# Kernel tuning notes

Measured on AMD Instinct MI355X. Metric: run time of the kernel, lower is better.

## Reference

```python
import jax, jax.numpy as jnp
import numpy as np

HEADS = 8
DIM_HEAD = 64
DIM = 512
KERNEL = 33
SCALE = DIM_HEAD ** -0.5


def setup_inputs() -> dict:
    key = jax.random.key(0)
    k1, k2, k3, k4, k5, k6 = jax.random.split(key, 6)
    b, n = 2, 2048
    inner = HEADS * DIM_HEAD
    x = jax.random.normal(k1, (b, n, DIM), dtype=jnp.float32)
    mask = jax.random.uniform(k2, (b, n)) < 0.9
    W_qkv = jax.random.normal(k3, (DIM, inner * 3), dtype=jnp.float32) / np.sqrt(DIM)
    W_out = jax.random.normal(k4, (inner, DIM), dtype=jnp.float32) / np.sqrt(inner)
    b_out = jax.random.normal(k5, (DIM,), dtype=jnp.float32) * 0.01
    # depthwise Conv2d(heads, heads, (K,1), groups=heads) weight: (O=heads, I/groups=1, K, 1)
    conv_w = jax.random.normal(k6, (HEADS, 1, KERNEL, 1), dtype=jnp.float32) / np.sqrt(KERNEL)
    return {"x": x, "mask": mask, "W_qkv": W_qkv, "W_out": W_out,
            "b_out": b_out, "conv_w": conv_w}


def reference(x, mask, W_qkv, W_out, b_out, conv_w):
    b, n, _ = x.shape
    h, d = HEADS, DIM_HEAD
    qkv = (x @ W_qkv).reshape(b, n, 3, h, d)          # chunk(3) then (h d) split
    q = qkv[:, :, 0].transpose(0, 2, 1, 3)            # b h n d
    k = qkv[:, :, 1].transpose(0, 2, 1, 3)
    v = qkv[:, :, 2].transpose(0, 2, 1, 3)
    dots = jnp.einsum('bhid,bhjd->bhij', q, k) * SCALE
    mask_value = -jnp.finfo(dots.dtype).max
    dots = jnp.where(mask[:, None, None, :], dots, mask_value)
    attn = jax.nn.softmax(dots, axis=-1)
    out = jnp.einsum('bhij,bhjd->bhid', attn, v)      # b h n d
    # depthwise residual conv over sequence axis (height), per head
    pad = KERNEL // 2
    res = jax.lax.conv_general_dilated(
        v, conv_w, window_strides=(1, 1), padding=((pad, pad), (0, 0)),
        dimension_numbers=('NCHW', 'OIHW', 'NCHW'), feature_group_count=h)
    out = out + res
    out = out.transpose(0, 2, 1, 3).reshape(b, n, h * d)  # b n (h d)
    out = out @ W_out + b_out
    out = jnp.where(mask[:, :, None], out, 0.0)
    return out
```

## Files before the change

### kernel.cpp

```cpp
#include <hip/hip_runtime.h>
#include <float.h>

#define BATCH 2
#define SEQ   2048
#define HEADS 8
#define DHEAD 64
#define DIMM  512
#define NQKV  1536
#define QSCALE_L2 (0.125f * 1.44269504f)

#define QKV_ELEMS ((size_t)BATCH * HEADS * SEQ * DHEAD)

typedef __bf16 bf16x8 __attribute__((ext_vector_type(8)));
typedef short  s16x4  __attribute__((ext_vector_type(4)));
typedef float  f32x4  __attribute__((ext_vector_type(4)));

#if __has_builtin(__builtin_amdgcn_exp2f)
#define EXP2F __builtin_amdgcn_exp2f
#else
#define EXP2F exp2f
#endif

__device__ __forceinline__ unsigned short bfbits(float f) {
  __bf16 h = (__bf16)f;
  return *(unsigned short*)&h;
}
__device__ __forceinline__ float bf2f(unsigned short u) {
  return __uint_as_float((unsigned)u << 16);
}
__device__ __forceinline__ unsigned cvtpk(float a, float b) {
  unsigned r;
  asm("v_cvt_pk_bf16_f32 %0, %1, %2" : "=v"(r) : "v"(a), "v"(b));
  return r;
}
__device__ __forceinline__ f32x4 mfma16(s16x4 a, s16x4 b, f32x4 c) {
#if __has_builtin(__builtin_amdgcn_mfma_f32_16x16x16bf16_1k)
  return __builtin_amdgcn_mfma_f32_16x16x16bf16_1k(a, b, c, 0, 0, 0);
#else
  f32x4 d;
  asm("v_mfma_f32_16x16x16_bf16 %0, %1, %2, %3" : "=v"(d) : "v"(a), "v"(b), "v"(c));
  return d;
#endif
}

__device__ __forceinline__ void transpose_tile_dev(
    const float* __restrict__ W, unsigned short* __restrict__ Wt,
    int K, int N, int n0, int k0, int t, float T[64][65]) {
  {
    int r0 = t >> 4, c4 = t & 15;
#pragma unroll
    for (int rr = 0; rr < 4; ++rr) {
      int r = r0 + rr * 16;
      float4 v = *(const float4*)(W + (size_t)(k0 + r) * N + n0 + c4 * 4);
      T[r][c4 * 4 + 0] = v.x; T[r][c4 * 4 + 1] = v.y;
      T[r][c4 * 4 + 2] = v.z; T[r][c4 * 4 + 3] = v.w;
    }
  }
  __syncthreads();
  {
    int n = t >> 2, kc = t & 3;
    union { unsigned short u[16]; int4 v[2]; } p;
#pragma unroll
    for (int i = 0; i < 16; ++i) p.u[i] = bfbits(T[kc * 16 + i][n]);
    int4* dst = (int4*)(Wt + (size_t)(n0 + n) * K + k0 + kc * 16);
    dst[0] = p.v[0]; dst[1] = p.v[1];
  }
}

__global__ __launch_bounds__(256) void prep_all(
    const float* __restrict__ X, const void* __restrict__ mraw,
    const float* __restrict__ Wqkv, const float* __restrict__ Wout,
    unsigned short* __restrict__ Xbf, float* __restrict__ maskf,
    unsigned short* __restrict__ Wtq, unsigned short* __restrict__ Wto,
    unsigned* __restrict__ kmaxn) {
  __shared__ float T[64][65];
  __shared__ int f_bf16, f_f32, f_gt1, f_oddnz;
  const int b = blockIdx.x;
  const int t = threadIdx.x;
  if (b < 1024) {
    size_t i = ((size_t)b * 256 + t) * 8;
    float4 a0 = *(const float4*)(X + i);
    float4 a1 = *(const float4*)(X + i + 4);
    union { unsigned short u[8]; int4 v; } pk;
    pk.u[0] = bfbits(a0.x); pk.u[1] = bfbits(a0.y);
    pk.u[2] = bfbits(a0.z); pk.u[3] = bfbits(a0.w);
    pk.u[4] = bfbits(a1.x); pk.u[5] = bfbits(a1.y);
    pk.u[6] = bfbits(a1.z); pk.u[7] = bfbits(a1.w);
    *(int4*)(Xbf + i) = pk.v;
  } else if (b < 1216) {
    int bb2 = b - 1024;
    transpose_tile_dev(Wqkv, Wtq, DIMM, NQKV, (bb2 % 24) * 64, (bb2 / 24) * 64, t, T);
  } else if (b < 1280) {
    int bb2 = b - 1216;
    transpose_tile_dev(Wout, Wto, DIMM, DIMM, (bb2 & 7) * 64, (bb2 >> 3) * 64, t, T);
  } else {
    if (t < 16) kmaxn[t] = 0u;
    if (t == 0) { f_bf16 = 0; f_f32 = 0; f_gt1 = 0; f_oddnz = 0; }
    __syncthreads();
    const unsigned int* w = (const unsigned int*)mraw;
    unsigned int v = w[t];
    if (v == 0x3f803f80u) f_bf16 = 1;
    if (v == 0x3f800000u) f_f32 = 1;
    if (v > 1u)           f_gt1 = 1;
    if ((t & 1) && v != 0u) f_oddnz = 1;
    __syncthreads();
    int mode;
    if (f_bf16)       mode = 4;
    else if (f_f32)   mode = 3;
    else if (f_gt1)   mode = 1;
    else if (!f_oddnz) mode = 2;
    else              mode = 0;
    for (int i = t; i < BATCH * SEQ; i += 256) {
      bool keep;
      if (mode == 4)      keep = ((const unsigned short*)mraw)[i] != 0;
      else if (mode == 3) keep = ((const float*)mraw)[i] != 0.f;
      else if (mode == 1) keep = ((const unsigned char*)mraw)[i] != 0;
      else if (mode == 2) keep = w[2 * i] != 0u;
      else                keep = w[i] != 0u;
      maskf[i] = keep ? 1.f : 0.f;
    }
  }
}

__global__ __launch_bounds__(256) void gemm_qkv_mfma(
    const unsigned short* __restrict__ Xbf, const unsigned short* __restrict__ Wt,
    unsigned short* __restrict__ Qbf, unsigned short* __restrict__ Kbf,
    unsigned short* __restrict__ Vt, unsigned* __restrict__ kmaxn) {
  __shared__ __align__(16) unsigned char Al[128 * 128];
  __shared__ __align__(16) unsigned char Bl[64 * 128];
  const int tid = threadIdx.x;
  const int lane = tid & 63;
  const int w = tid >> 6;
  const int l15 = lane & 15, g = lane >> 4;
  const int wr = w >> 1, wc = w & 1;
  int bid = blockIdx.x;
  int lid = (bid & 7) * 96 + (bid >> 3);
  int by = lid / 24, bx = lid - by * 24;
  const int m0 = by * 128;

  f32x4 acc[4][2] = {};
  const int srow = tid >> 3, scg = tid & 7;
  const int rsw = (l15 & 7) << 4;

  for (int k0 = 0; k0 < DIMM; k0 += 64) {
    __syncthreads();
#pragma unroll
    for (int it = 0; it < 4; ++it) {
      int row = srow + it * 32;
      int sw = (row & 7) << 4;
      *(int4*)(Al + row * 128 + ((scg * 16) ^ sw)) =
          *(const int4*)(Xbf + (size_t)(m0 + row) * DIMM + k0 + scg * 8);
      if (it < 2) {
        *(int4*)(Bl + row * 128 + ((scg * 16) ^ sw)) =
            *(const int4*)(Wt + (size_t)(bx * 64 + row) * DIMM + k0 + scg * 8);
      }
    }
    __syncthreads();
#pragma unroll
    for (int ks = 0; ks < 2; ++ks) {
      bf16x8 af[4], bfr[2];
#pragma unroll
      for (int mi = 0; mi < 4; ++mi)
        af[mi] = *(const bf16x8*)(Al + (wr * 64 + mi * 16 + l15) * 128 +
                                  ((ks * 64 + g * 16) ^ rsw));
#pragma unroll
      for (int nj = 0; nj < 2; ++nj)
        bfr[nj] = *(const bf16x8*)(Bl + (wc * 32 + nj * 16 + l15) * 128 +
                                   ((ks * 64 + g * 16) ^ rsw));
#pragma unroll
      for (int mi = 0; mi < 4; ++mi)
#pragma unroll
        for (int nj = 0; nj < 2; ++nj)
          acc[mi][nj] = __builtin_amdgcn_mfma_f32_16x16x32_bf16(
              af[mi], bfr[nj], acc[mi][nj], 0, 0, 0);
    }
  }
  const int chunk = bx >> 3;
  const int bb = m0 >> 11;
#pragma unroll
  for (int nj = 0; nj < 2; ++nj) {
    int col = (bx & 7) * 64 + wc * 32 + nj * 16 + l15;
    int hh = col >> 6, dd = col & 63;
#pragma unroll
    for (int mi = 0; mi < 4; ++mi) {
      int ii0 = (m0 & (SEQ - 1)) + wr * 64 + mi * 16 + g * 4;
      if (chunk == 2) {
        union { unsigned short u[4]; ushort4 v; } pk;
#pragma unroll
        for (int r = 0; r < 4; ++r) pk.u[r] = bfbits(acc[mi][nj][r]);
        *(ushort4*)(Vt + ((size_t)(bb * HEADS + hh) * DHEAD + dd) * SEQ + ii0) = pk.v;
      } else {
        unsigned short* dst = (chunk == 0) ? Qbf : Kbf;
        float sc = (chunk == 0) ? QSCALE_L2 : 1.f;
#pragma unroll
        for (int r = 0; r < 4; ++r)
          dst[((size_t)(bb * HEADS + hh) * SEQ + ii0 + r) * DHEAD + dd] =
              bfbits(acc[mi][nj][r] * sc);
      }
    }
  }
  if (chunk == 1) {
    float kab = 0.f;
#pragma unroll
    for (int nj = 0; nj < 2; ++nj)
#pragma unroll
      for (int mi = 0; mi < 4; ++mi)
#pragma unroll
        for (int r = 0; r < 4; ++r) kab = fmaxf(kab, fabsf(acc[mi][nj][r]));
#pragma unroll
    for (int d = 1; d < 64; d <<= 1) kab = fmaxf(kab, __shfl_xor(kab, d));
    if (lane == 0)
      atomicMax(kmaxn + (bb * HEADS + (bx & 7)), __float_as_uint(kab * 1.005f));
  }
}

__global__ __launch_bounds__(256) void attn_split(const unsigned short* __restrict__ Qbf,
                                                  const unsigned short* __restrict__ Kbf,
                                                  const unsigned short* __restrict__ Vt,
                                                  const float* __restrict__ maskf,
                                                  const unsigned* __restrict__ kmaxn,
                                                  unsigned short* __restrict__ Po,
                                                  float* __restrict__ LSE) {
  __shared__ __align__(16) unsigned char Ks[16384];
  __shared__ __align__(16) unsigned char Vs[16384];

  const int tid = threadIdx.x;
  const int lane = tid & 63;
  const int w = tid >> 6;
  const int l15 = lane & 15, g = lane >> 4;

  int fid = blockIdx.x;
  int lid = (fid & 7) * 128 + (fid >> 3);
  const int bh = lid >> 6;
  const int rem = lid & 63;
  const int qb = rem >> 1;
  const int half = rem & 1;
  const int bb = bh >> 3;

  const unsigned short* Qg = Qbf + ((size_t)bh * SEQ + qb * 64) * DHEAD;
  const unsigned short* Kg = Kbf + (size_t)bh * SEQ * DHEAD;
  const unsigned short* Vg = Vt  + (size_t)bh * DHEAD * SEQ;
  const float* mrow = maskf + bb * SEQ;

  bf16x8 qf0, qf1;
  {
    const unsigned char* qrow = (const unsigned char*)(Qg + (size_t)(w * 16 + l15) * DHEAD);
    qf0 = *(const bf16x8*)(qrow + g * 16);
    qf1 = *(const bf16x8*)(qrow + 64 + g * 16);
  }
  float Bx, Bnat;
  {
    float qn2 = 0.f;
#pragma unroll
    for (int i = 0; i < 8; ++i) {
      float a = (float)qf0[i]; qn2 += a * a;
      float b = (float)qf1[i]; qn2 += b * b;
    }
    qn2 += __shfl_xor(qn2, 16);
    qn2 += __shfl_xor(qn2, 32);
    const float kabs = __uint_as_float(kmaxn[bh]);
    Bx = sqrtf(qn2) * 8.f * kabs;
    Bnat = Bx * 0.69314718f;
  }

  f32x4 o[4] = {};
  float lsum = 0.f;

  const int sm = tid >> 2;
  const int sc = (tid & 3) * 32;
  const int ssw = (sm & 7) << 4;
  const int rsw = (l15 & 7) << 4;
  const int kt0 = half * 16;

  int4 rk0, rk1, rv0, rv1;
  {
    const unsigned char* ksrc =
        (const unsigned char*)(Kg + (size_t)kt0 * 64 * DHEAD) + sm * 128 + sc;
    const unsigned char* vsrc =
        (const unsigned char*)(Vg + (size_t)sm * SEQ + kt0 * 64) + sc;
    rk0 = *(const int4*)(ksrc); rk1 = *(const int4*)(ksrc + 16);
    rv0 = *(const int4*)(vsrc); rv1 = *(const int4*)(vsrc + 16);
  }
  *(int4*)(Ks + sm * 128 + ((sc)      ^ ssw)) = rk0;
  *(int4*)(Ks + sm * 128 + ((sc + 16) ^ ssw)) = rk1;
  *(int4*)(Vs + sm * 128 + ((sc)      ^ ssw)) = rv0;
  *(int4*)(Vs + sm * 128 + ((sc + 16) ^ ssw)) = rv1;
  __syncthreads();

  for (int t = 0; t < 16; ++t) {
    const int kt = kt0 + t;
    const int co = (t & 1) << 13;
    const int no = co ^ 8192;
    float4 km[4];
#pragma unroll
    for (int j = 0; j < 4; ++j) km[j] = *(const float4*)(mrow + kt * 64 + 16 * j + 4 * g);
    if (t < 15) {
      const unsigned char* ksrc =
          (const unsigned char*)(Kg + (size_t)(kt + 1) * 64 * DHEAD) + sm * 128 + sc;
      const unsigned char* vsrc =
          (const unsigned char*)(Vg + (size_t)sm * SEQ + (kt + 1) * 64) + sc;
      rk0 = *(const int4*)(ksrc); rk1 = *(const int4*)(ksrc + 16);
      rv0 = *(const int4*)(vsrc); rv1 = *(const int4*)(vsrc + 16);
    }

    f32x4 s[4];
#pragma unroll
    for (int j = 0; j < 4; ++j) {
      const unsigned char* krow = Ks + co + (16 * j + l15) * 128;
      bf16x8 kf0 = *(const bf16x8*)(krow + ((g * 16)      ^ rsw));
      bf16x8 kf1 = *(const bf16x8*)(krow + ((64 + g * 16) ^ rsw));
      f32x4 z = (f32x4){0.f, 0.f, 0.f, 0.f};
      z = __builtin_amdgcn_mfma_f32_16x16x32_bf16(kf0, qf0, z, 0, 0, 0);
      z = __builtin_amdgcn_mfma_f32_16x16x32_bf16(kf1, qf1, z, 0, 0, 0);
      s[j] = z;
    }

    s16x4 pa[4];
#pragma unroll
    for (int j = 0; j < 4; ++j) {
      float p0 = EXP2F(s[j][0] - Bx) * km[j].x;
      float p1 = EXP2F(s[j][1] - Bx) * km[j].y;
      float p2 = EXP2F(s[j][2] - Bx) * km[j].z;
      float p3 = EXP2F(s[j][3] - Bx) * km[j].w;
      lsum += (p0 + p1) + (p2 + p3);
      union { uint2 u; s16x4 v; } pk;
      pk.u.x = cvtpk(p0, p1);
      pk.u.y = cvtpk(p2, p3);
      pa[j] = pk.v;
    }

#pragma unroll
    for (int dj = 0; dj < 4; ++dj) {
      const unsigned char* vrow = Vs + co + (16 * dj + l15) * 128;
#pragma unroll
      for (int j = 0; j < 4; ++j) {
        s16x4 vb = *(const s16x4*)(vrow + ((32 * j + 8 * g) ^ rsw));
        o[dj] = mfma16(pa[j], vb, o[dj]);
      }
    }

    if (t < 15) {
      *(int4*)(Ks + no + sm * 128 + ((sc)      ^ ssw)) = rk0;
      *(int4*)(Ks + no + sm * 128 + ((sc + 16) ^ ssw)) = rk1;
      *(int4*)(Vs + no + sm * 128 + ((sc)      ^ ssw)) = rv0;
      *(int4*)(Vs + no + sm * 128 + ((sc + 16) ^ ssw)) = rv1;
      __syncthreads();
    }
  }

  lsum += __shfl_xor(lsum, 16);
  lsum += __shfl_xor(lsum, 32);
#pragma unroll
  for (int r = 0; r < 4; ++r) {
    float lr = __shfl(lsum, 4 * g + r);
    float inv = (lr > 0.f) ? 1.f / lr : 0.f;
    int row = qb * 64 + w * 16 + 4 * g + r;
    size_t base = half * QKV_ELEMS + ((size_t)bh * SEQ + row) * DHEAD + l15;
    Po[base]      = bfbits(o[0][r] * inv);
    Po[base + 16] = bfbits(o[1][r] * inv);
    Po[base + 32] = bfbits(o[2][r] * inv);
    Po[base + 48] = bfbits(o[3][r] * inv);
  }
  if (g == 0) {
    int row = qb * 64 + w * 16 + l15;
    LSE[half * (BATCH * HEADS * SEQ) + bh * SEQ + row] =
        (lsum > 0.f) ? Bnat + __logf(lsum) : -3.0e38f;
  }
}

__global__ __launch_bounds__(256) void combine_conv(
    const unsigned short* __restrict__ Po, const float* __restrict__ LSE,
    const unsigned short* __restrict__ Vt, const float* __restrict__ cw,
    unsigned short* __restrict__ Obf) {
  __shared__ float T[96][68];
  __shared__ float cwl[33];
  const int tid = threadIdx.x;
  const int bid = blockIdx.x;
  const int bh = bid >> 5;
  const int n0 = (bid & 31) * 64;
  const int hh = bh & 7;
  if (tid < 33) cwl[tid] = cw[hh * 33 + tid];
  for (int idx = tid; idx < 64 * 24; idx += 256) {
    int d = idx / 24, c4 = idx - (idx / 24) * 24;
    int nbase = n0 - 16 + c4 * 4;
    const unsigned short* src = Vt + ((size_t)bh * DHEAD + d) * SEQ;
#pragma unroll
    for (int q = 0; q < 4; ++q) {
      int n = nbase + q;
      T[c4 * 4 + q][d] = (n >= 0 && n < SEQ) ? bf2f(src[n]) : 0.f;
    }
  }
  __syncthreads();
#pragma unroll
  for (int p = 0; p < 4; ++p) {
    int n = (tid >> 4) + p * 16;
    int d4 = tid & 15;
    int row = bh * SEQ + n0 + n;
    float ls0 = LSE[row], ls1 = LSE[BATCH * HEADS * SEQ + row];
    float m = fmaxf(ls0, ls1);
    float w0 = __expf(ls0 - m), w1 = __expf(ls1 - m);
    float inv = 1.f / (w0 + w1);
    w0 *= inv; w1 *= inv;
    const unsigned short* p0 = Po + (size_t)row * DHEAD + d4 * 4;
    const unsigned short* p1 = p0 + QKV_ELEMS;
    ushort4 a = *(const ushort4*)p0, b = *(const ushort4*)p1;
    float o0 = w0 * bf2f(a.x) + w1 * bf2f(b.x);
    float o1 = w0 * bf2f(a.y) + w1 * bf2f(b.y);
    float o2 = w0 * bf2f(a.z) + w1 * bf2f(b.z);
    float o3 = w0 * bf2f(a.w) + w1 * bf2f(b.w);
#pragma unroll
    for (int t = 0; t < 33; ++t) {
      float wv = cwl[t];
      float4 tv = *(const float4*)&T[n + t][d4 * 4];
      o0 += wv * tv.x; o1 += wv * tv.y; o2 += wv * tv.z; o3 += wv * tv.w;
    }
    union { unsigned short u[4]; ushort4 v; } pk;
    pk.u[0] = bfbits(o0); pk.u[1] = bfbits(o1);
    pk.u[2] = bfbits(o2); pk.u[3] = bfbits(o3);
    *(ushort4*)(Obf + (size_t)row * DHEAD + d4 * 4) = pk.v;
  }
}

__global__ __launch_bounds__(256) void gemm_out_mfma(
    const unsigned short* __restrict__ Obf, const unsigned short* __restrict__ Wt,
    const float* __restrict__ bias, const float* __restrict__ maskf,
    float* __restrict__ out) {
  __shared__ __align__(16) unsigned char Al[64 * 128];
  __shared__ __align__(16) unsigned char Bl[64 * 128];
  const int tid = threadIdx.x;
  const int lane = tid & 63;
  const int w = tid >> 6;
  const int l15 = lane & 15, g = lane >> 4;
  const int wr = w >> 1, wc = w & 1;
  int bid = blockIdx.x;
  int lid = (bid & 7) * 64 + (bid >> 3);
  int by = lid >> 3, bx = lid & 7;
  const int m0 = by * 64, n0 = bx * 64;
  const int bb = m0 >> 11;
  const int ii0 = m0 & (SEQ - 1);

  f32x4 acc[2][2] = {};
  const int srow = tid >> 3, scg = tid & 7;
  const int rsw = (l15 & 7) << 4;

  for (int k0 = 0; k0 < DIMM; k0 += 64) {
    const int hh = k0 >> 6;
    __syncthreads();
#pragma unroll
    for (int it = 0; it < 2; ++it) {
      int row = srow + it * 32;
      int sw = (row & 7) << 4;
      *(int4*)(Al + row * 128 + ((scg * 16) ^ sw)) =
          *(const int4*)(Obf + ((size_t)(bb * HEADS + hh) * SEQ + ii0 + row) * DHEAD + scg * 8);
      *(int4*)(Bl + row * 128 + ((scg * 16) ^ sw)) =
          *(const int4*)(Wt + (size_t)(n0 + row) * DIMM + k0 + scg * 8);
    }
    __syncthreads();
#pragma unroll
    for (int ks = 0; ks < 2; ++ks) {
      bf16x8 af[2], bfr[2];
#pragma unroll
      for (int mi = 0; mi < 2; ++mi)
        af[mi] = *(const bf16x8*)(Al + (wr * 32 + mi * 16 + l15) * 128 +
                                  ((ks * 64 + g * 16) ^ rsw));
#pragma unroll
      for (int nj = 0; nj < 2; ++nj)
        bfr[nj] = *(const bf16x8*)(Bl + (wc * 32 + nj * 16 + l15) * 128 +
                                   ((ks * 64 + g * 16) ^ rsw));
#pragma unroll
      for (int mi = 0; mi < 2; ++mi)
#pragma unroll
        for (int nj = 0; nj < 2; ++nj)
          acc[mi][nj] = __builtin_amdgcn_mfma_f32_16x16x32_bf16(
              af[mi], bfr[nj], acc[mi][nj], 0, 0, 0);
    }
  }
#pragma unroll
  for (int nj = 0; nj < 2; ++nj) {
    int col = n0 + wc * 32 + nj * 16 + l15;
    float bcol = bias[col];
#pragma unroll
    for (int mi = 0; mi < 2; ++mi) {
#pragma unroll
      for (int r = 0; r < 4; ++r) {
        int m = m0 + wr * 32 + mi * 16 + g * 4 + r;
        out[(size_t)m * DIMM + col] = (acc[mi][nj][r] + bcol) * maskf[m];
      }
    }
  }
}

extern "C" void kernel_launch(void* const* d_in, const int* in_sizes, int n_in,
                              void* d_out, int out_size, void* d_ws, size_t ws_size,
                              hipStream_t stream) {
  const float* x     = (const float*)d_in[0];
  const void*  mask  = d_in[1];
  const float* Wqkv  = (const float*)d_in[2];
  const float* Wout  = (const float*)d_in[3];
  const float* bout  = (const float*)d_in[4];
  const float* convw = (const float*)d_in[5];
  float* out = (float*)d_out;

  float* maskf = (float*)d_ws;
  unsigned* kmaxn = (unsigned*)(maskf + 4096);
  unsigned short* Qbf = (unsigned short*)(kmaxn + 64);
  unsigned short* Kbf = Qbf + QKV_ELEMS;
  unsigned short* Vt  = Kbf + QKV_ELEMS;
  unsigned short* Po  = Vt + QKV_ELEMS;
  float* LSE          = (float*)(Po + 2 * QKV_ELEMS);
  unsigned short* Obf = (unsigned short*)(LSE + 2 * BATCH * HEADS * SEQ);
  unsigned short* Wtq = Obf + QKV_ELEMS;
  unsigned short* Wto = Wtq + (size_t)NQKV * DIMM;
  unsigned short* Xbf = Wto + (size_t)DIMM * DIMM;

  prep_all<<<1281, 256, 0, stream>>>(x, mask, Wqkv, Wout, Xbf, maskf, Wtq, Wto, kmaxn);
  gemm_qkv_mfma<<<768, 256, 0, stream>>>(Xbf, Wtq, Qbf, Kbf, Vt, kmaxn);
  attn_split<<<1024, 256, 0, stream>>>(Qbf, Kbf, Vt, maskf, kmaxn, Po, LSE);
  combine_conv<<<512, 256, 0, stream>>>(Po, LSE, Vt, convw, Obf);
  gemm_out_mfma<<<512, 256, 0, stream>>>(Obf, Wto, bout, maskf, out);
}
```

Before: 100.4 us.

## Split attention KV range four ways and add V LDS bank swizzle

```diff
diff --git a/kernel.cpp b/kernel.cpp
--- a/kernel.cpp
+++ b/kernel.cpp
@@ -10,6 +10,8 @@
 #define QSCALE_L2 (0.125f * 1.44269504f)
 
 #define QKV_ELEMS ((size_t)BATCH * HEADS * SEQ * DHEAD)
+#define BHS (BATCH * HEADS * SEQ)
+#define NSPLIT 4
 
 typedef __bf16 bf16x8 __attribute__((ext_vector_type(8)));
 typedef short  s16x4  __attribute__((ext_vector_type(4)));
@@ -230,11 +232,11 @@
   const int l15 = lane & 15, g = lane >> 4;
 
   int fid = blockIdx.x;
-  int lid = (fid & 7) * 128 + (fid >> 3);
-  const int bh = lid >> 6;
-  const int rem = lid & 63;
-  const int qb = rem >> 1;
-  const int half = rem & 1;
+  int lid = (fid & 7) * 256 + (fid >> 3);
+  const int bh = lid >> 7;
+  const int rem = lid & 127;
+  const int qb = rem >> 2;
+  const int quarter = rem & 3;
   const int bb = bh >> 3;
 
   const unsigned short* Qg = Qbf + ((size_t)bh * SEQ + qb * 64) * DHEAD;
@@ -269,8 +271,10 @@
   const int sm = tid >> 2;
   const int sc = (tid & 3) * 32;
   const int ssw = (sm & 7) << 4;
+  const int vswap = (sm >> 3) & 1;
   const int rsw = (l15 & 7) << 4;
-  const int kt0 = half * 16;
+  const int vsw = rsw | (((l15 >> 3) & 1) << 3);
+  const int kt0 = quarter * 8;
 
   int4 rk0, rk1, rv0, rv1;
   {
@@ -281,20 +285,24 @@
     rk0 = *(const int4*)(ksrc); rk1 = *(const int4*)(ksrc + 16);
     rv0 = *(const int4*)(vsrc); rv1 = *(const int4*)(vsrc + 16);
   }
-  *(int4*)(Ks + sm * 128 + ((sc)      ^ ssw)) = rk0;
-  *(int4*)(Ks + sm * 128 + ((sc + 16) ^ ssw)) = rk1;
-  *(int4*)(Vs + sm * 128 + ((sc)      ^ ssw)) = rv0;
-  *(int4*)(Vs + sm * 128 + ((sc + 16) ^ ssw)) = rv1;
+  {
+    *(int4*)(Ks + sm * 128 + ((sc)      ^ ssw)) = rk0;
+    *(int4*)(Ks + sm * 128 + ((sc + 16) ^ ssw)) = rk1;
+    int4 sv0 = vswap ? (int4){rv0.z, rv0.w, rv0.x, rv0.y} : rv0;
+    int4 sv1 = vswap ? (int4){rv1.z, rv1.w, rv1.x, rv1.y} : rv1;
+    *(int4*)(Vs + sm * 128 + ((sc)      ^ ssw)) = sv0;
+    *(int4*)(Vs + sm * 128 + ((sc + 16) ^ ssw)) = sv1;
+  }
   __syncthreads();
 
-  for (int t = 0; t < 16; ++t) {
+  for (int t = 0; t < 8; ++t) {
     const int kt = kt0 + t;
     const int co = (t & 1) << 13;
     const int no = co ^ 8192;
     float4 km[4];
 #pragma unroll
     for (int j = 0; j < 4; ++j) km[j] = *(const float4*)(mrow + kt * 64 + 16 * j + 4 * g);
-    if (t < 15) {
+    if (t < 7) {
       const unsigned char* ksrc =
           (const unsigned char*)(Kg + (size_t)(kt + 1) * 64 * DHEAD) + sm * 128 + sc;
       const unsigned char* vsrc =
@@ -334,16 +342,18 @@
       const unsigned char* vrow = Vs + co + (16 * dj + l15) * 128;
 #pragma unroll
       for (int j = 0; j < 4; ++j) {
-        s16x4 vb = *(const s16x4*)(vrow + ((32 * j + 8 * g) ^ rsw));
+        s16x4 vb = *(const s16x4*)(vrow + ((32 * j + 8 * g) ^ vsw));
         o[dj] = mfma16(pa[j], vb, o[dj]);
       }
     }
 
-    if (t < 15) {
+    if (t < 7) {
       *(int4*)(Ks + no + sm * 128 + ((sc)      ^ ssw)) = rk0;
       *(int4*)(Ks + no + sm * 128 + ((sc + 16) ^ ssw)) = rk1;
-      *(int4*)(Vs + no + sm * 128 + ((sc)      ^ ssw)) = rv0;
-      *(int4*)(Vs + no + sm * 128 + ((sc + 16) ^ ssw)) = rv1;
+      int4 sv0 = vswap ? (int4){rv0.z, rv0.w, rv0.x, rv0.y} : rv0;
+      int4 sv1 = vswap ? (int4){rv1.z, rv1.w, rv1.x, rv1.y} : rv1;
+      *(int4*)(Vs + no + sm * 128 + ((sc)      ^ ssw)) = sv0;
+      *(int4*)(Vs + no + sm * 128 + ((sc + 16) ^ ssw)) = sv1;
       __syncthreads();
     }
   }
@@ -355,7 +365,7 @@
     float lr = __shfl(lsum, 4 * g + r);
     float inv = (lr > 0.f) ? 1.f / lr : 0.f;
     int row = qb * 64 + w * 16 + 4 * g + r;
-    size_t base = half * QKV_ELEMS + ((size_t)bh * SEQ + row) * DHEAD + l15;
+    size_t base = (size_t)quarter * QKV_ELEMS + ((size_t)bh * SEQ + row) * DHEAD + l15;
     Po[base]      = bfbits(o[0][r] * inv);
     Po[base + 16] = bfbits(o[1][r] * inv);
     Po[base + 32] = bfbits(o[2][r] * inv);
@@ -363,7 +373,7 @@
   }
   if (g == 0) {
     int row = qb * 64 + w * 16 + l15;
-    LSE[half * (BATCH * HEADS * SEQ) + bh * SEQ + row] =
+    LSE[quarter * BHS + bh * SEQ + row] =
         (lsum > 0.f) ? Bnat + __logf(lsum) : -3.0e38f;
   }
 }
@@ -396,18 +406,21 @@
     int n = (tid >> 4) + p * 16;
     int d4 = tid & 15;
     int row = bh * SEQ + n0 + n;
-    float ls0 = LSE[row], ls1 = LSE[BATCH * HEADS * SEQ + row];
-    float m = fmaxf(ls0, ls1);
-    float w0 = __expf(ls0 - m), w1 = __expf(ls1 - m);
-    float inv = 1.f / (w0 + w1);
-    w0 *= inv; w1 *= inv;
-    const unsigned short* p0 = Po + (size_t)row * DHEAD + d4 * 4;
-    const unsigned short* p1 = p0 + QKV_ELEMS;
-    ushort4 a = *(const ushort4*)p0, b = *(const ushort4*)p1;
-    float o0 = w0 * bf2f(a.x) + w1 * bf2f(b.x);
-    float o1 = w0 * bf2f(a.y) + w1 * bf2f(b.y);
-    float o2 = w0 * bf2f(a.z) + w1 * bf2f(b.z);
-    float o3 = w0 * bf2f(a.w) + w1 * bf2f(b.w);
+    float ls[NSPLIT], m = -3.0e38f;
+#pragma unroll
+    for (int q = 0; q < NSPLIT; ++q) { ls[q] = LSE[q * BHS + row]; m = fmaxf(m, ls[q]); }
+    float wq[NSPLIT], tot = 0.f;
+#pragma unroll
+    for (int q = 0; q < NSPLIT; ++q) { wq[q] = __expf(ls[q] - m); tot += wq[q]; }
+    float inv = 1.f / tot;
+    float o0 = 0.f, o1 = 0.f, o2 = 0.f, o3 = 0.f;
+#pragma unroll
+    for (int q = 0; q < NSPLIT; ++q) {
+      float wk = wq[q] * inv;
+      ushort4 a = *(const ushort4*)(Po + (size_t)q * QKV_ELEMS + (size_t)row * DHEAD + d4 * 4);
+      o0 += wk * bf2f(a.x); o1 += wk * bf2f(a.y);
+      o2 += wk * bf2f(a.z); o3 += wk * bf2f(a.w);
+    }
 #pragma unroll
     for (int t = 0; t < 33; ++t) {
       float wv = cwl[t];
@@ -507,15 +520,15 @@
   unsigned short* Kbf = Qbf + QKV_ELEMS;
   unsigned short* Vt  = Kbf + QKV_ELEMS;
   unsigned short* Po  = Vt + QKV_ELEMS;
-  float* LSE          = (float*)(Po + 2 * QKV_ELEMS);
-  unsigned short* Obf = (unsigned short*)(LSE + 2 * BATCH * HEADS * SEQ);
+  float* LSE          = (float*)(Po + NSPLIT * QKV_ELEMS);
+  unsigned short* Obf = (unsigned short*)(LSE + NSPLIT * BHS);
   unsigned short* Wtq = Obf + QKV_ELEMS;
   unsigned short* Wto = Wtq + (size_t)NQKV * DIMM;
   unsigned short* Xbf = Wto + (size_t)DIMM * DIMM;
 
   prep_all<<<1281, 256, 0, stream>>>(x, mask, Wqkv, Wout, Xbf, maskf, Wtq, Wto, kmaxn);
   gemm_qkv_mfma<<<768, 256, 0, stream>>>(Xbf, Wtq, Qbf, Kbf, Vt, kmaxn);
-  attn_split<<<1024, 256, 0, stream>>>(Qbf, Kbf, Vt, maskf, kmaxn, Po, LSE);
+  attn_split<<<2048, 256, 0, stream>>>(Qbf, Kbf, Vt, maskf, kmaxn, Po, LSE);
   combine_conv<<<512, 256, 0, stream>>>(Po, LSE, Vt, convw, Obf);
   gemm_out_mfma<<<512, 256, 0, stream>>>(Obf, Wto, bout, maskf, out);
 }
```

New measurement: 99.55 us. Within noise of the previous version (-0.9%).
